# Performance work log

Measured on AMD Instinct MI355X. Metric: run time of the kernel, lower is better.

## Reference

```python
import jax, jax.numpy as jnp
import numpy as np

K = 4
C = 512
CLAMP = (1e-4, 1.0 - 1e-4)
INIT_ALPHAS = (0.8, 0.9, 0.98, 0.99)


def setup_inputs() -> dict:
    key = jax.random.key(0)
    kx, = jax.random.split(key, 1)
    B, T = 16, 4096
    x = jax.random.normal(kx, (B, T, C), dtype=jnp.float32)
    # logit_alpha: [K, C], each row initialized to logit(alpha_k)
    alphas = np.clip(np.array(INIT_ALPHAS[:K], dtype=np.float32), CLAMP[0], CLAMP[1])
    logit = np.log(alphas / (1.0 - alphas))  # logit
    logit_alpha = jnp.asarray(np.repeat(logit[:, None], C, axis=1), dtype=jnp.float32)
    mix_logits = jnp.zeros((C, K), dtype=jnp.float32)
    return {"x": x, "logit_alpha": logit_alpha, "mix_logits": mix_logits}


def reference(x, logit_alpha, mix_logits):
    # x: [B, T, C]; logit_alpha: [K, C]; mix_logits: [C, K]
    B, T, Cc = x.shape
    x32 = x.astype(jnp.float32)
    a = jnp.clip(jax.nn.sigmoid(logit_alpha.astype(jnp.float32)), CLAMP[0], CLAMP[1])  # [K, C]
    one_minus_a = 1.0 - a

    y0 = jnp.broadcast_to(x32[:, 0, None, :], (B, K, Cc))  # [B, K, C]

    def step(y_prev, xt):  # y_prev: [B,K,C], xt: [B,C]
        y = a * y_prev + one_minus_a * xt[:, None, :]
        return y, y

    xs = jnp.swapaxes(x32[:, 1:, :], 0, 1)  # [T-1, B, C]
    _, ys = jax.lax.scan(step, y0, xs)  # ys: [T-1, B, K, C]
    yk_all = jnp.concatenate([y0[None], ys], axis=0)  # [T, B, K, C]

    mix = jax.nn.softmax(mix_logits.astype(jnp.float32), axis=-1)  # [C, K]
    trend = jnp.einsum('tbkc,ck->btc', yk_all, mix)
    return trend.astype(x.dtype)
```

## Files before the change

kernel.cpp:

```cpp
#include <hip/hip_runtime.h>

#define B_  16
#define T_  4096
#define C_  512
#define K_  4
#define NT_ 64
#define L_  (T_ / NT_)
#define C4_ (C_ / 4)

typedef float nfloat4 __attribute__((ext_vector_type(4)));

__device__ __forceinline__ float sigmoid_clamp(float la) {
    float av = 1.0f / (1.0f + expf(-la));
    return fminf(fmaxf(av, 1e-4f), 1.0f - 1e-4f);
}

__global__ __launch_bounds__(256) void ema_pass1(const float4* __restrict__ x4,
                                                 const float* __restrict__ logit_alpha,
                                                 float4* __restrict__ ws4) {
    const int c4 = threadIdx.x & (C4_ - 1);
    const int jh = threadIdx.x >> 7;
    const int b  = blockIdx.x / (NT_ / 2);
    const int j  = (blockIdx.x % (NT_ / 2)) * 2 + jh;

    float4 a[K_], oma[K_], s[K_];
#pragma unroll
    for (int k = 0; k < K_; ++k) {
        float4 la = ((const float4*)logit_alpha)[k * C4_ + c4];
        a[k].x = sigmoid_clamp(la.x); a[k].y = sigmoid_clamp(la.y);
        a[k].z = sigmoid_clamp(la.z); a[k].w = sigmoid_clamp(la.w);
        oma[k].x = 1.0f - a[k].x; oma[k].y = 1.0f - a[k].y;
        oma[k].z = 1.0f - a[k].z; oma[k].w = 1.0f - a[k].w;
        s[k].x = s[k].y = s[k].z = s[k].w = 0.0f;
    }

    const float4* xp = x4 + ((size_t)b * T_ + (size_t)j * L_) * C4_ + c4;
#pragma unroll 4
    for (int i = 0; i < L_; ++i) {
        float4 xv = xp[(size_t)i * C4_];
#pragma unroll
        for (int k = 0; k < K_; ++k) {
            s[k].x = fmaf(a[k].x, s[k].x, oma[k].x * xv.x);
            s[k].y = fmaf(a[k].y, s[k].y, oma[k].y * xv.y);
            s[k].z = fmaf(a[k].z, s[k].z, oma[k].z * xv.z);
            s[k].w = fmaf(a[k].w, s[k].w, oma[k].w * xv.w);
        }
    }

#pragma unroll
    for (int k = 0; k < K_; ++k)
        ws4[(((size_t)b * K_ + k) * NT_ + j) * C4_ + c4] = s[k];
}

__global__ __launch_bounds__(128) void ema_pass2(const float* __restrict__ x,
                                                 const float* __restrict__ logit_alpha,
                                                 float* __restrict__ ws) {
    const int ct = blockIdx.x & 3;
    const int bk = blockIdx.x >> 2;
    const int b  = bk / K_;
    const int k  = bk % K_;
    const int c  = ct * 128 + threadIdx.x;

    float av = sigmoid_clamp(logit_alpha[k * C_ + c]);
    float A = av;
#pragma unroll
    for (int q = 0; q < 6; ++q) A *= A;

    float carry = x[(size_t)b * T_ * C_ + c];
    float* wsb = ws + ((size_t)b * K_ + k) * NT_ * C_ + c;
    for (int j = 0; j < NT_; ++j) {
        float sj = wsb[(size_t)j * C_];
        wsb[(size_t)j * C_] = carry;
        carry = fmaf(A, carry, sj);
    }
}

__global__ __launch_bounds__(256) void ema_pass3(const float4* __restrict__ x4,
                                                 const float* __restrict__ logit_alpha,
                                                 const float4* __restrict__ ml4,
                                                 const float4* __restrict__ ws4,
                                                 float4* __restrict__ out4) {
    const int c4 = threadIdx.x & (C4_ - 1);
    const int jh = threadIdx.x >> 7;
    const int b  = blockIdx.x / (NT_ / 2);
    const int j  = (blockIdx.x % (NT_ / 2)) * 2 + jh;

    float4 a[K_], oma[K_], y[K_];
    float  m[K_][4];
#pragma unroll
    for (int k = 0; k < K_; ++k) {
        float4 la = ((const float4*)logit_alpha)[k * C4_ + c4];
        a[k].x = sigmoid_clamp(la.x); a[k].y = sigmoid_clamp(la.y);
        a[k].z = sigmoid_clamp(la.z); a[k].w = sigmoid_clamp(la.w);
        oma[k].x = 1.0f - a[k].x; oma[k].y = 1.0f - a[k].y;
        oma[k].z = 1.0f - a[k].z; oma[k].w = 1.0f - a[k].w;
        y[k] = ws4[(((size_t)b * K_ + k) * NT_ + j) * C4_ + c4];
    }

#pragma unroll
    for (int ci = 0; ci < 4; ++ci) {
        float4 ml = ml4[(size_t)c4 * 4 + ci];
        float mx = fmaxf(fmaxf(ml.x, ml.y), fmaxf(ml.z, ml.w));
        float e0 = expf(ml.x - mx), e1 = expf(ml.y - mx);
        float e2 = expf(ml.z - mx), e3 = expf(ml.w - mx);
        float inv = 1.0f / (e0 + e1 + e2 + e3);
        m[0][ci] = e0 * inv; m[1][ci] = e1 * inv;
        m[2][ci] = e2 * inv; m[3][ci] = e3 * inv;
    }

    const float4* xp = x4   + ((size_t)b * T_ + (size_t)j * L_) * C4_ + c4;
    float4*       op = out4 + ((size_t)b * T_ + (size_t)j * L_) * C4_ + c4;
#pragma unroll 4
    for (int i = 0; i < L_; ++i) {
        float4 xv = xp[(size_t)i * C4_];
        float4 acc; acc.x = acc.y = acc.z = acc.w = 0.0f;
#pragma unroll
        for (int k = 0; k < K_; ++k) {
            y[k].x = fmaf(a[k].x, y[k].x, oma[k].x * xv.x);
            y[k].y = fmaf(a[k].y, y[k].y, oma[k].y * xv.y);
            y[k].z = fmaf(a[k].z, y[k].z, oma[k].z * xv.z);
            y[k].w = fmaf(a[k].w, y[k].w, oma[k].w * xv.w);
            acc.x = fmaf(m[k][0], y[k].x, acc.x);
            acc.y = fmaf(m[k][1], y[k].y, acc.y);
            acc.z = fmaf(m[k][2], y[k].z, acc.z);
            acc.w = fmaf(m[k][3], y[k].w, acc.w);
        }
        nfloat4 nv = { acc.x, acc.y, acc.z, acc.w };
        __builtin_nontemporal_store(nv, (nfloat4*)&op[(size_t)i * C4_]);
    }
}

extern "C" void kernel_launch(void* const* d_in, const int* in_sizes, int n_in,
                              void* d_out, int out_size, void* d_ws, size_t ws_size,
                              hipStream_t stream) {
    const float* x           = (const float*)d_in[0];
    const float* logit_alpha = (const float*)d_in[1];
    const float* mix_logits  = (const float*)d_in[2];
    float* out = (float*)d_out;
    float* ws  = (float*)d_ws;

    ema_pass1<<<B_ * NT_ / 2, 256, 0, stream>>>((const float4*)x, logit_alpha,
                                                (float4*)ws);
    ema_pass2<<<B_ * K_ * 4, 128, 0, stream>>>(x, logit_alpha, ws);
    ema_pass3<<<B_ * NT_ / 2, 256, 0, stream>>>((const float4*)x, logit_alpha,
                                                (const float4*)mix_logits,
                                                (const float4*)ws, (float4*)out);
}
```

Baseline: 75.71 us.

## Stage a bf16 copy of x in workspace for the third pass

Pass 1 now streams x with nontemporal loads and also writes a bf16-rounded copy of it into the workspace. Pass 3 reads that half-width copy instead of re-reading the fp32 input. The partial-sum region moves to an offset after the bf16 buffer, and the old fp32 kernels are kept as a fallback when the workspace is too small. The intent is to cut pass-3 read traffic, but pass 1 gains an extra write, so total bytes moved stay about the same. It also adds bf16 rounding error to the recurrence input.

```diff
diff --git a/kernel.cpp b/kernel.cpp
--- a/kernel.cpp
+++ b/kernel.cpp
@@ -8,16 +8,30 @@
 #define L_  (T_ / NT_)
 #define C4_ (C_ / 4)
 
-typedef float nfloat4 __attribute__((ext_vector_type(4)));
+#define WS_BF16_BYTES  ((size_t)B_ * T_ * C_ * 2)
+#define WS_PART_FLTS   (WS_BF16_BYTES / 4)
+#define WS_NEEDED      (WS_BF16_BYTES + (size_t)B_ * K_ * NT_ * C_ * 4)
+
+typedef float  nfloat4  __attribute__((ext_vector_type(4)));
+typedef unsigned short nushort4 __attribute__((ext_vector_type(4)));
 
 __device__ __forceinline__ float sigmoid_clamp(float la) {
     float av = 1.0f / (1.0f + expf(-la));
     return fminf(fmaxf(av, 1e-4f), 1.0f - 1e-4f);
 }
 
+__device__ __forceinline__ unsigned short f32_to_bf16_rne(float f) {
+    unsigned int u = __float_as_uint(f);
+    u += 0x7fffu + ((u >> 16) & 1u);
+    return (unsigned short)(u >> 16);
+}
+__device__ __forceinline__ float bf16_to_f32(unsigned short h) {
+    return __uint_as_float(((unsigned int)h) << 16);
+}
+
 __global__ __launch_bounds__(256) void ema_pass1(const float4* __restrict__ x4,
                                                  const float* __restrict__ logit_alpha,
-                                                 float4* __restrict__ ws4) {
+                                                 float* __restrict__ ws) {
     const int c4 = threadIdx.x & (C4_ - 1);
     const int jh = threadIdx.x >> 7;
     const int b  = blockIdx.x / (NT_ / 2);
@@ -34,10 +48,14 @@
         s[k].x = s[k].y = s[k].z = s[k].w = 0.0f;
     }
 
-    const float4* xp = x4 + ((size_t)b * T_ + (size_t)j * L_) * C4_ + c4;
-#pragma unroll 4
-    for (int i = 0; i < L_; ++i) {
-        float4 xv = xp[(size_t)i * C4_];
+    const nfloat4* xp = (const nfloat4*)x4 + ((size_t)b * T_ + (size_t)j * L_) * C4_ + c4;
+    nushort4* bp = (nushort4*)ws + ((size_t)b * T_ + (size_t)j * L_) * C4_ + c4;
+#pragma unroll 4
+    for (int i = 0; i < L_; ++i) {
+        nfloat4 xv = __builtin_nontemporal_load(&xp[(size_t)i * C4_]);
+        nushort4 hb = { f32_to_bf16_rne(xv.x), f32_to_bf16_rne(xv.y),
+                        f32_to_bf16_rne(xv.z), f32_to_bf16_rne(xv.w) };
+        bp[(size_t)i * C4_] = hb;
 #pragma unroll
         for (int k = 0; k < K_; ++k) {
             s[k].x = fmaf(a[k].x, s[k].x, oma[k].x * xv.x);
@@ -47,6 +65,7 @@
         }
     }
 
+    float4* ws4 = (float4*)(ws + WS_PART_FLTS);
 #pragma unroll
     for (int k = 0; k < K_; ++k)
         ws4[(((size_t)b * K_ + k) * NT_ + j) * C4_ + c4] = s[k];
@@ -54,7 +73,7 @@
 
 __global__ __launch_bounds__(128) void ema_pass2(const float* __restrict__ x,
                                                  const float* __restrict__ logit_alpha,
-                                                 float* __restrict__ ws) {
+                                                 float* __restrict__ wsp) {
     const int ct = blockIdx.x & 3;
     const int bk = blockIdx.x >> 2;
     const int b  = bk / K_;
@@ -67,7 +86,7 @@
     for (int q = 0; q < 6; ++q) A *= A;
 
     float carry = x[(size_t)b * T_ * C_ + c];
-    float* wsb = ws + ((size_t)b * K_ + k) * NT_ * C_ + c;
+    float* wsb = wsp + ((size_t)b * K_ + k) * NT_ * C_ + c;
     for (int j = 0; j < NT_; ++j) {
         float sj = wsb[(size_t)j * C_];
         wsb[(size_t)j * C_] = carry;
@@ -75,10 +94,9 @@
     }
 }
 
-__global__ __launch_bounds__(256) void ema_pass3(const float4* __restrict__ x4,
+__global__ __launch_bounds__(256) void ema_pass3(const float* __restrict__ ws,
                                                  const float* __restrict__ logit_alpha,
                                                  const float4* __restrict__ ml4,
-                                                 const float4* __restrict__ ws4,
                                                  float4* __restrict__ out4) {
     const int c4 = threadIdx.x & (C4_ - 1);
     const int jh = threadIdx.x >> 7;
@@ -87,6 +105,7 @@
 
     float4 a[K_], oma[K_], y[K_];
     float  m[K_][4];
+    const float4* ws4 = (const float4*)(ws + WS_PART_FLTS);
 #pragma unroll
     for (int k = 0; k < K_; ++k) {
         float4 la = ((const float4*)logit_alpha)[k * C4_ + c4];
@@ -108,6 +127,96 @@
         m[2][ci] = e2 * inv; m[3][ci] = e3 * inv;
     }
 
+    const nushort4* bp = (const nushort4*)ws + ((size_t)b * T_ + (size_t)j * L_) * C4_ + c4;
+    float4*         op = out4 + ((size_t)b * T_ + (size_t)j * L_) * C4_ + c4;
+#pragma unroll 4
+    for (int i = 0; i < L_; ++i) {
+        nushort4 hb = bp[(size_t)i * C4_];
+        float xx = bf16_to_f32(hb.x), xy = bf16_to_f32(hb.y);
+        float xz = bf16_to_f32(hb.z), xw = bf16_to_f32(hb.w);
+        float4 acc; acc.x = acc.y = acc.z = acc.w = 0.0f;
+#pragma unroll
+        for (int k = 0; k < K_; ++k) {
+            y[k].x = fmaf(a[k].x, y[k].x, oma[k].x * xx);
+            y[k].y = fmaf(a[k].y, y[k].y, oma[k].y * xy);
+            y[k].z = fmaf(a[k].z, y[k].z, oma[k].z * xz);
+            y[k].w = fmaf(a[k].w, y[k].w, oma[k].w * xw);
+            acc.x = fmaf(m[k][0], y[k].x, acc.x);
+            acc.y = fmaf(m[k][1], y[k].y, acc.y);
+            acc.z = fmaf(m[k][2], y[k].z, acc.z);
+            acc.w = fmaf(m[k][3], y[k].w, acc.w);
+        }
+        nfloat4 nv = { acc.x, acc.y, acc.z, acc.w };
+        __builtin_nontemporal_store(nv, (nfloat4*)&op[(size_t)i * C4_]);
+    }
+}
+
+__global__ __launch_bounds__(256) void ema_pass1_f32(const float4* __restrict__ x4,
+                                                     const float* __restrict__ logit_alpha,
+                                                     float4* __restrict__ ws4) {
+    const int c4 = threadIdx.x & (C4_ - 1);
+    const int jh = threadIdx.x >> 7;
+    const int b  = blockIdx.x / (NT_ / 2);
+    const int j  = (blockIdx.x % (NT_ / 2)) * 2 + jh;
+
+    float4 a[K_], oma[K_], s[K_];
+#pragma unroll
+    for (int k = 0; k < K_; ++k) {
+        float4 la = ((const float4*)logit_alpha)[k * C4_ + c4];
+        a[k].x = sigmoid_clamp(la.x); a[k].y = sigmoid_clamp(la.y);
+        a[k].z = sigmoid_clamp(la.z); a[k].w = sigmoid_clamp(la.w);
+        oma[k].x = 1.0f - a[k].x; oma[k].y = 1.0f - a[k].y;
+        oma[k].z = 1.0f - a[k].z; oma[k].w = 1.0f - a[k].w;
+        s[k].x = s[k].y = s[k].z = s[k].w = 0.0f;
+    }
+    const float4* xp = x4 + ((size_t)b * T_ + (size_t)j * L_) * C4_ + c4;
+#pragma unroll 4
+    for (int i = 0; i < L_; ++i) {
+        float4 xv = xp[(size_t)i * C4_];
+#pragma unroll
+        for (int k = 0; k < K_; ++k) {
+            s[k].x = fmaf(a[k].x, s[k].x, oma[k].x * xv.x);
+            s[k].y = fmaf(a[k].y, s[k].y, oma[k].y * xv.y);
+            s[k].z = fmaf(a[k].z, s[k].z, oma[k].z * xv.z);
+            s[k].w = fmaf(a[k].w, s[k].w, oma[k].w * xv.w);
+        }
+    }
+#pragma unroll
+    for (int k = 0; k < K_; ++k)
+        ws4[(((size_t)b * K_ + k) * NT_ + j) * C4_ + c4] = s[k];
+}
+
+__global__ __launch_bounds__(256) void ema_pass3_f32(const float4* __restrict__ x4,
+                                                     const float* __restrict__ logit_alpha,
+                                                     const float4* __restrict__ ml4,
+                                                     const float4* __restrict__ ws4,
+                                                     float4* __restrict__ out4) {
+    const int c4 = threadIdx.x & (C4_ - 1);
+    const int jh = threadIdx.x >> 7;
+    const int b  = blockIdx.x / (NT_ / 2);
+    const int j  = (blockIdx.x % (NT_ / 2)) * 2 + jh;
+
+    float4 a[K_], oma[K_], y[K_];
+    float  m[K_][4];
+#pragma unroll
+    for (int k = 0; k < K_; ++k) {
+        float4 la = ((const float4*)logit_alpha)[k * C4_ + c4];
+        a[k].x = sigmoid_clamp(la.x); a[k].y = sigmoid_clamp(la.y);
+        a[k].z = sigmoid_clamp(la.z); a[k].w = sigmoid_clamp(la.w);
+        oma[k].x = 1.0f - a[k].x; oma[k].y = 1.0f - a[k].y;
+        oma[k].z = 1.0f - a[k].z; oma[k].w = 1.0f - a[k].w;
+        y[k] = ws4[(((size_t)b * K_ + k) * NT_ + j) * C4_ + c4];
+    }
+#pragma unroll
+    for (int ci = 0; ci < 4; ++ci) {
+        float4 ml = ml4[(size_t)c4 * 4 + ci];
+        float mx = fmaxf(fmaxf(ml.x, ml.y), fmaxf(ml.z, ml.w));
+        float e0 = expf(ml.x - mx), e1 = expf(ml.y - mx);
+        float e2 = expf(ml.z - mx), e3 = expf(ml.w - mx);
+        float inv = 1.0f / (e0 + e1 + e2 + e3);
+        m[0][ci] = e0 * inv; m[1][ci] = e1 * inv;
+        m[2][ci] = e2 * inv; m[3][ci] = e3 * inv;
+    }
     const float4* xp = x4   + ((size_t)b * T_ + (size_t)j * L_) * C4_ + c4;
     float4*       op = out4 + ((size_t)b * T_ + (size_t)j * L_) * C4_ + c4;
 #pragma unroll 4
@@ -139,10 +248,18 @@
     float* out = (float*)d_out;
     float* ws  = (float*)d_ws;
 
-    ema_pass1<<<B_ * NT_ / 2, 256, 0, stream>>>((const float4*)x, logit_alpha,
-                                                (float4*)ws);
-    ema_pass2<<<B_ * K_ * 4, 128, 0, stream>>>(x, logit_alpha, ws);
-    ema_pass3<<<B_ * NT_ / 2, 256, 0, stream>>>((const float4*)x, logit_alpha,
-                                                (const float4*)mix_logits,
-                                                (const float4*)ws, (float4*)out);
-}
+    if (ws_size >= WS_NEEDED) {
+        ema_pass1<<<B_ * NT_ / 2, 256, 0, stream>>>((const float4*)x, logit_alpha, ws);
+        ema_pass2<<<B_ * K_ * 4, 128, 0, stream>>>(x, logit_alpha, ws + WS_PART_FLTS);
+        ema_pass3<<<B_ * NT_ / 2, 256, 0, stream>>>(ws, logit_alpha,
+                                                    (const float4*)mix_logits,
+                                                    (float4*)out);
+    } else {
+        ema_pass1_f32<<<B_ * NT_ / 2, 256, 0, stream>>>((const float4*)x, logit_alpha,
+                                                        (float4*)ws);
+        ema_pass2<<<B_ * K_ * 4, 128, 0, stream>>>(x, logit_alpha, ws);
+        ema_pass3_f32<<<B_ * NT_ / 2, 256, 0, stream>>>((const float4*)x, logit_alpha,
+                                                        (const float4*)mix_logits,
+                                                        (const float4*)ws, (float4*)out);
+    }
+}
```

Measured after the change: 82.39 us. 1.09x slower.
